# Performance work log

Measured on AMD Instinct MI355X. Metric: run time of the kernel, lower is better.

Reference implementation:

```python
import jax, jax.numpy as jnp
from jax import lax
import numpy as np

B, T = 8, 16
IMG = 128
CF = 32            # c_CNN_out = dim_C2_2 (feature channels / NTM slot width)
WO = HO = 32       # w_CNN_out, h_CNN_out
N = WO * HO        # dim_C2_1 = NTM memory slots (flattened spatial)
M = CF
DH = 256           # dim_h_o
LAMBDA0 = 1e-4
EPS = 1e-8


def setup_inputs() -> dict:
    key = jax.random.key(0)
    ks = jax.random.split(key, 12)
    f32 = jnp.float32
    inp = {}
    inp["x_i"] = jax.random.normal(ks[0], (B, T, 3, IMG, IMG), f32)
    inp["z_i"] = jax.random.normal(ks[1], (B, T, 3, IMG, IMG), f32)
    # feature CNN (3 -> CF -> CF, stride 2 each)
    inp["conv1_w"] = jax.random.normal(ks[2], (CF, 3, 3, 3), f32) * 0.1
    inp["conv1_b"] = jnp.zeros((CF,), f32)
    inp["conv2_w"] = jax.random.normal(ks[3], (CF, CF, 3, 3), f32) * 0.05
    inp["conv2_b"] = jnp.zeros((CF,), f32)
    # NTM controller / addressing parameters
    inp["Wk"] = jax.random.normal(ks[4], (M, DH), f32) * 0.05
    inp["bk"] = jnp.zeros((M,), f32)
    inp["Wbeta"] = jax.random.normal(ks[5], (1, DH), f32) * 0.05
    inp["bbeta"] = jnp.zeros((1,), f32)
    inp["Wh"] = jax.random.normal(ks[6], (DH, DH + 2 * M), f32) * 0.05
    inp["bh"] = jnp.zeros((DH,), f32)
    inp["We"] = jax.random.normal(ks[7], (M, DH), f32) * 0.05
    inp["Wa"] = jax.random.normal(ks[8], (M, DH), f32) * 0.05
    inp["Wg"] = jax.random.normal(ks[9], (1, DH), f32) * 0.05
    # DCF cosine window and gaussian-label FFT (stored as real/imag pair like torch.rfft)
    win = np.hanning(WO)
    inp["cos_window"] = jnp.asarray(np.outer(win, win), f32)
    sigma = 2.0
    g = np.arange(WO)
    g = np.minimum(g, WO - g)  # circular distance, peak at origin
    d2 = g[:, None] ** 2 + g[None, :] ** 2
    y = np.exp(-d2 / (2.0 * sigma ** 2)).astype(np.float32)
    yfc = np.fft.rfft2(y)
    inp["yf"] = jnp.asarray(np.stack([yfc.real, yfc.imag], -1), f32)[None, None]  # [1,1,WO,WO//2+1,2]
    return inp


def _conv(x, w, b):
    out = lax.conv_general_dilated(x, w, (2, 2), "SAME",
                                   dimension_numbers=("NCHW", "OIHW", "NCHW"))
    return out + b[None, :, None, None]


def _feature(x, c1w, c1b, c2w, c2b):
    x = jax.nn.relu(_conv(x, c1w, c1b))
    return jax.nn.relu(_conv(x, c2w, c2b))  # [BT, CF, WO, HO]


def _layernorm(x):
    # LayerNorm over last two dims [dim_C2_1, dim_C2_2], no affine
    mu = x.mean(axis=(-2, -1), keepdims=True)
    var = x.var(axis=(-2, -1), keepdims=True)
    return (x - mu) / jnp.sqrt(var + 1e-5)


def reference(x_i, z_i, conv1_w, conv1_b, conv2_w, conv2_b,
              Wk, bk, Wbeta, bbeta, Wh, bh, We, Wa, Wg, cos_window, yf):
    # feature extraction
    xf_btcwh = _feature(x_i.reshape(B * T, 3, IMG, IMG), conv1_w, conv1_b, conv2_w, conv2_b)
    zf_btcwh = _feature(z_i.reshape(B * T, 3, IMG, IMG), conv1_w, conv1_b, conv2_w, conv2_b)
    xf = xf_btcwh.transpose(0, 2, 3, 1).reshape(B, T, N, M)  # [B,T,N,M]

    h0 = jnp.zeros((B, DH), xf.dtype)
    c0 = _layernorm(xf[:, 0])  # init_x_norm on first frame features

    def cell(carry, x_t):
        h, c = carry  # h [B,DH], c [B,N,M]; x_t [B,N,M]
        # content-based addressing
        k = jnp.tanh(h @ Wk.T + bk)                           # [B,M]
        beta = jax.nn.softplus(h @ Wbeta.T + bbeta)           # [B,1]
        cn = c / (jnp.linalg.norm(c, axis=-1, keepdims=True) + EPS)
        kn = k / (jnp.linalg.norm(k, axis=-1, keepdims=True) + EPS)
        sims = jnp.einsum("bnm,bm->bn", cn, kn)               # cosine sim [B,N]
        w = jax.nn.softmax(beta * sims, axis=-1)              # read/write weights
        r = jnp.einsum("bn,bnm->bm", w, c)                    # read vector
        # controller update
        inp = jnp.concatenate([h, r, x_t.mean(axis=1)], axis=-1)  # [B,DH+2M]
        h_new = jnp.tanh(inp @ Wh.T + bh)
        # erase / add / input-gate write
        e = jax.nn.sigmoid(h_new @ We.T)                      # [B,M]
        a = jnp.tanh(h_new @ Wa.T)                            # [B,M]
        g = jax.nn.sigmoid(h_new @ Wg.T)[:, :, None]          # [B,1,1]
        c_write = c * (1.0 - w[:, :, None] * e[:, None, :]) + w[:, :, None] * a[:, None, :]
        c_new = (1.0 - g) * c_write + g * x_t
        return (h_new, c_new), c_new

    (_, _), c_seq = lax.scan(cell, (h0, c0), xf.transpose(1, 0, 2, 3))
    c_seq = c_seq.transpose(1, 0, 2, 3)                       # [B,T,N,M]

    # c.permute(0,1,3,2).view(B*T, dim_C2_2, WO, HO)
    c_btcwh = c_seq.transpose(0, 1, 3, 2).reshape(B * T, M, WO, HO)

    # DCF correlation in Fourier domain
    cw = cos_window[None, None]
    cfft = jnp.fft.rfft2(c_btcwh * cw)                        # [BT,M,WO,WO//2+1]
    zfft = jnp.fft.rfft2(zf_btcwh * cw)
    kzzf = (cfft.real ** 2 + cfft.imag ** 2).sum(axis=1, keepdims=True)   # [BT,1,WO,Wf]
    kxzf = (zfft * jnp.conj(cfft)).sum(axis=1, keepdims=True)             # complex_mulconj sum
    yfc = yf[..., 0] + 1j * yf[..., 1]                         # [1,1,WO,Wf]
    alphaf = yfc / (kzzf + LAMBDA0)
    response = jnp.fft.irfft2(kxzf * alphaf, s=(WO, HO))       # [BT,1,WO,HO]
    return response.reshape(B, T, WO, HO)
```

## Files before the change

kernel.cpp:

```cpp
#include <hip/hip_runtime.h>
#include <hip/hip_fp16.h>
#include <math.h>


#define TWOPI_32 0.19634954084936207f

typedef _Float16 __h2 __attribute__((ext_vector_type(2)));
__device__ __forceinline__ float fdot2(unsigned int w, unsigned int h, float acc) {
    union { unsigned int u; __h2 v; } a, b;
    a.u = w; b.u = h;
    return __builtin_amdgcn_fdot2(a.v, b.v, acc, false);
}
__device__ __forceinline__ unsigned int packh2(float a, float b) {
    __half2 h2 = __floats2half2_rn(a, b);
    return *(unsigned int*)&h2;
}

__global__ __launch_bounds__(256) void prepack_kernel(
    const float* __restrict__ Wh, const float* __restrict__ Wk,
    const float* __restrict__ We, const float* __restrict__ Wa,
    const float* __restrict__ c1w, const float* __restrict__ c2w,
    __half* __restrict__ whhP, __half* __restrict__ whrxP,
    __half* __restrict__ wkP, __half* __restrict__ weP, __half* __restrict__ waP,
    float* __restrict__ twg,
    unsigned int* __restrict__ c2wP, unsigned int* __restrict__ c1wP01,
    float* __restrict__ c1wP2)
{
    const int tid = threadIdx.x;
    if (blockIdx.x < 32) {
        const int base = blockIdx.x*256 + tid;
        #pragma unroll
        for (int r = 0; r < 8; ++r) {
            int idx = base*8 + r;
            int e = idx & 7, i = (idx >> 3) & 255, c = idx >> 11;
            int q = c >> 4, k = c & 15;
            whhP[idx] = __float2half(Wh[i*320 + q*128 + k*8 + e]);
        }
        #pragma unroll
        for (int r = 0; r < 2; ++r) {
            int idx = base*2 + r;
            int i = idx >> 6, s2 = idx & 63;
            whrxP[idx] = __float2half(Wh[i*320 + 256 + s2]);
        }
        {
            int idx = base;
            int m = idx >> 8, j = (idx >> 4) & 15, e = idx & 15;
            int col = (e < 8) ? (8*j + e) : (128 + 8*j + (e - 8));
            wkP[idx] = __float2half(Wk[m*256 + col]);
            weP[idx] = __float2half(We[m*256 + col]);
            waP[idx] = __float2half(Wa[m*256 + col]);
        }
    } else {
        for (int idx = tid; idx < 4608; idx += 256) {
            int half = idx / 2304;
            int rem  = idx - half*2304;
            int ic2  = rem / 144;
            int r2   = rem - ic2*144;
            int j    = r2 / 9, q = r2 - j*9;
            int oc   = half*16 + j;
            c2wP[((half*16 + ic2)*16 + j)*12 + q] =
                packh2(c2w[oc*288 + (2*ic2)*9 + q],
                       c2w[oc*288 + (2*ic2+1)*9 + q]);
        }
        for (int idx = tid; idx < 288; idx += 256) {
            int oc = idx / 9, r = idx - oc*9;
            c1wP01[idx] = packh2(c1w[oc*27 + r*3 + 0], c1w[oc*27 + r*3 + 1]);
            c1wP2[idx]  = c1w[oc*27 + r*3 + 2];
        }
        for (int idx = tid; idx < 1024; idx += 256) {
            int w = idx >> 5, k = idx & 31;
            float sv, cv;
            sincosf(TWOPI_32 * (float)((w*k) & 31), &sv, &cv);
            twg[idx*2]     = cv;
            twg[idx*2 + 1] = -sv;
        }
    }
}

__global__ __launch_bounds__(256) void conv1_kernel(const float* __restrict__ in,
                                                    const unsigned int* __restrict__ w01,
                                                    const float* __restrict__ w2,
                                                    const float* __restrict__ bias,
                                                    unsigned int* __restrict__ out)
{
    const int strip = blockIdx.x;
    const int img   = blockIdx.y;
    const int tid   = threadIdx.x;
    __shared__ __align__(16) unsigned int sIn2[3*33*66];
    __shared__ unsigned int sw01[288];
    __shared__ float sw2[288];
    __shared__ float sb[32];
    for (int i = tid; i < 288; i += 256) { sw01[i] = w01[i]; sw2[i] = w2[i]; }
    if (tid < 32) sb[tid] = bias[tid];
    const int iy0 = strip * 32;
    for (int idx = tid; idx < 3*33*66; idx += 256) {
        int ic  = idx / (33*66);
        int rem = idx - ic*(33*66);
        int li  = rem / 66;
        int x2  = rem - li*66;
        int iy  = iy0 + li;
        unsigned int v = 0;
        if (iy < 128 && x2 < 64) {
            float2 p = *(const float2*)&in[(((size_t)img*3 + ic)*128 + iy)*128 + 2*x2];
            v = packh2(p.x, p.y);
        }
        sIn2[idx] = v;
    }
    __syncthreads();
    const int oy0 = strip*16;
    #pragma unroll
    for (int p = 0; p < 4; ++p) {
        int pos = p*256 + tid;
        int ly = pos >> 6;
        int ox = pos & 63;
        unsigned int pa[9];
        float px[9];
        #pragma unroll
        for (int ic = 0; ic < 3; ++ic)
            #pragma unroll
            for (int dy = 0; dy < 3; ++dy) {
                int r = ic*3 + dy;
                int rowb = ic*(33*66) + (2*ly+dy)*66;
                pa[r] = sIn2[rowb + ox];
                unsigned int u = sIn2[rowb + ox + 1];
                px[r] = __half2float(((const __half2*)&u)->x);
            }
        for (int oc2 = 0; oc2 < 16; ++oc2) {
            const int oca = 2*oc2, ocb = 2*oc2 + 1;
            float acca = sb[oca], accb = sb[ocb];
            #pragma unroll
            for (int r = 0; r < 9; ++r) {
                acca = fdot2(sw01[oca*9 + r], pa[r], acca);
                acca += sw2[oca*9 + r] * px[r];
                accb = fdot2(sw01[ocb*9 + r], pa[r], accb);
                accb += sw2[ocb*9 + r] * px[r];
            }
            out[(((size_t)img*16 + oc2)*64 + (oy0+ly))*64 + ox] =
                packh2(fmaxf(acca, 0.f), fmaxf(accb, 0.f));
        }
    }
}

__global__ __launch_bounds__(256) void conv2_kernel(const unsigned int* __restrict__ in,
                                                    const unsigned int* __restrict__ wP,
                                                    const float* __restrict__ bias,
                                                    float* __restrict__ out)
{
    const int strip = blockIdx.x;
    const int img   = blockIdx.y;
    const int tid   = threadIdx.x;
    __shared__ __align__(16) unsigned int sIn2[16*9*66];
    __shared__ __align__(16) unsigned int sW[6144];
    __shared__ float sb[32];
    for (int i = tid; i < 1536; i += 256) ((uint4*)sW)[i] = ((const uint4*)wP)[i];
    if (tid < 32) sb[tid] = bias[tid];
    const int iy0 = strip*8;
    for (int idx = tid; idx < 16*9*66; idx += 256) {
        int ic2 = idx / (9*66);
        int rem = idx - ic2*(9*66);
        int li  = rem / 66;
        int col = rem - li*66;
        int iy  = iy0 + li;
        unsigned int v = 0;
        if (iy < 64 && col < 64)
            v = in[(((size_t)img*16 + ic2)*64 + iy)*64 + col];
        sIn2[idx] = v;
    }
    __syncthreads();
    const int posl = tid & 127;
    const int half = tid >> 7;
    const int ly = posl >> 5;
    const int ox = posl & 31;
    float acc[16];
    #pragma unroll
    for (int j = 0; j < 16; ++j) acc[j] = 0.f;
    for (int ic2 = 0; ic2 < 16; ++ic2) {
        unsigned int patch[9];
        #pragma unroll
        for (int dy = 0; dy < 3; ++dy)
            #pragma unroll
            for (int dx = 0; dx < 3; ++dx)
                patch[dy*3+dx] = sIn2[ic2*(9*66) + (2*ly+dy)*66 + 2*ox + dx];
        const unsigned int* wbase = sW + (half*16 + ic2)*192;
        #pragma unroll
        for (int j = 0; j < 16; ++j) {
            const unsigned int* wr = wbase + j*12;
            uint4 wa = *(const uint4*)wr;
            uint4 wb = *(const uint4*)(wr + 4);
            unsigned int w8 = wr[8];
            float a = acc[j];
            a = fdot2(wa.x, patch[0], a); a = fdot2(wa.y, patch[1], a);
            a = fdot2(wa.z, patch[2], a); a = fdot2(wa.w, patch[3], a);
            a = fdot2(wb.x, patch[4], a); a = fdot2(wb.y, patch[5], a);
            a = fdot2(wb.z, patch[6], a); a = fdot2(wb.w, patch[7], a);
            a = fdot2(w8,  patch[8], a);
            acc[j] = a;
        }
    }
    const int oy = strip*4 + ly;
    #pragma unroll
    for (int j = 0; j < 16; ++j) {
        int oc = half*16 + j;
        out[(((size_t)img*32 + oc)*32 + oy)*32 + ox] = fmaxf(acc[j] + sb[oc], 0.f);
    }
}

__global__ __launch_bounds__(256) void prep2_kernel(
    const float* __restrict__ xf, __half* __restrict__ xh, float* __restrict__ xmean)
{
    const int tid = threadIdx.x;
    const int bt = blockIdx.x;
    __shared__ float sT[32][257];
    const float* src = xf + (size_t)bt*32768;
    __half* dst = xh + (size_t)bt*32768;
    for (int tt = 0; tt < 4; ++tt) {
        #pragma unroll
        for (int m = 0; m < 32; ++m)
            sT[m][tid] = src[m*1024 + tt*256 + tid];
        __syncthreads();
        uint4 o[4];
        unsigned int* ou = (unsigned int*)o;
        #pragma unroll
        for (int k = 0; k < 16; ++k)
            ou[k] = packh2(sT[2*k][tid], sT[2*k+1][tid]);
        uint4* dp = (uint4*)(dst + (size_t)(tt*256 + tid)*32);
        dp[0] = o[0]; dp[1] = o[1]; dp[2] = o[2]; dp[3] = o[3];
        __syncthreads();
    }
    const int m = tid >> 3, s8 = tid & 7;
    float sm = 0.f;
    #pragma unroll 16
    for (int k = 0; k < 128; ++k) sm += src[m*1024 + s8 + 8*k];
    sm += __shfl_down(sm, 4, 8); sm += __shfl_down(sm, 2, 8); sm += __shfl_down(sm, 1, 8);
    if (s8 == 0) xmean[bt*32 + m] = sm * (1.f/1024.f);
}

__global__ __launch_bounds__(512, 2) void fat_kernel(
    const float* __restrict__ xfeat, const __half* __restrict__ xh,
    const float* __restrict__ xmean,
    const __half* __restrict__ whhP, const __half* __restrict__ whrxP,
    const __half* __restrict__ wkP, const __half* __restrict__ weP,
    const __half* __restrict__ waP,
    const float* __restrict__ bk, const float* __restrict__ Wbeta,
    const float* __restrict__ bbeta, const float* __restrict__ bh,
    const float* __restrict__ Wg,
    float* __restrict__ wbuf, float* __restrict__ eag, float* __restrict__ lnst,
    const float* __restrict__ z_i, const unsigned int* __restrict__ c1w01,
    const float* __restrict__ c1w2, const float* __restrict__ c1b,
    const unsigned int* __restrict__ c2wP, const float* __restrict__ c2b,
    float* __restrict__ zfeat)
{
    __shared__ __align__(16) char smem[139264];

    if (blockIdx.x < 8) {
        __half* sWhh = (__half*)(smem);
        float (*sHbuf)[256] = (float(*)[256])(smem + 131072);
        __half (*sHh)[256] = (__half(*)[256])(smem + 133120);
        float* sK    = (float*)(smem + 134144);
        float* sXm   = (float*)(smem + 134272);
        float* sRedC = (float*)(smem + 136320);
        float* sR32  = (float*)(smem + 137344);
        float* sE    = (float*)(smem + 137472);
        float* sA    = (float*)(smem + 137600);
        float* sBk   = (float*)(smem + 137728);
        float* sBh   = (float*)(smem + 137856);
        float* sRedD = (float*)(smem + 138880);
        float* sRedL = (float*)(smem + 138912);

        const int b    = blockIdx.x;
        const int tid  = threadIdx.x;
        const int lane = tid & 63;
        const int wid  = tid >> 6;

        {
            const uint4* src = (const uint4*)whhP;
            uint4* dst = (uint4*)sWhh;
            for (int i2 = tid; i2 < 8192; i2 += 512) dst[i2] = src[i2];
        }
        if (tid < 256) { sBh[tid] = bh[tid]; sHbuf[0][tid] = 0.f; sHh[0][tid] = __float2half(0.f); }
        if (tid < 32)  { sBk[tid] = bk[tid]; sK[tid] = tanhf(bk[tid]); }
        if (tid < 512) sXm[tid] = xmean[b*512 + tid];
        float4 wbeta4 = *(const float4*)&Wbeta[(size_t)lane*4];
        float4 wg4    = *(const float4*)&Wg[(size_t)lane*4];
        float bb = bbeta[0];

        const int mg = tid >> 4, jg = tid & 15;
        uint4 wk0, wk1, we0, we1, wa0, wa1;
        {
            const uint4* p;
            p = (const uint4*)(wkP + (size_t)(mg*16 + jg)*16); wk0 = p[0]; wk1 = p[1];
            p = (const uint4*)(weP + (size_t)(mg*16 + jg)*16); we0 = p[0]; we1 = p[1];
            p = (const uint4*)(waP + (size_t)(mg*16 + jg)*16); wa0 = p[0]; wa1 = p[1];
        }
        const int iD = tid >> 1, qD = tid & 1;
        uint4 wrx0, wrx1, wrx2, wrx3;
        {
            const uint4* p = (const uint4*)(whrxP + (size_t)iD*64 + qD*32);
            wrx0 = p[0]; wrx1 = p[1]; wrx2 = p[2]; wrx3 = p[3];
        }

        const int n0 = 2*tid;
        float c0[32], c1[32];

        {
            const float* x0 = xfeat + (size_t)(b*16)*32768;
            float sum = 0.f, ss = 0.f;
            #pragma unroll
            for (int m = 0; m < 32; ++m) {
                float2 v = *(const float2*)&x0[m*1024 + n0];
                c0[m] = v.x; c1[m] = v.y;
                sum += v.x + v.y; ss += v.x*v.x + v.y*v.y;
            }
            #pragma unroll
            for (int d = 32; d > 0; d >>= 1) { sum += __shfl_xor(sum, d, 64); ss += __shfl_xor(ss, d, 64); }
            if (lane == 0) { sRedL[wid] = sum; sRedL[8+wid] = ss; }
            __syncthreads();
            float S = 0.f, SS = 0.f;
            #pragma unroll
            for (int i = 0; i < 8; ++i) { S += sRedL[i]; SS += sRedL[8+i]; }
            float mu = S * (1.f/32768.f);
            float var = SS * (1.f/32768.f) - mu*mu;
            float rs = rsqrtf(var + 1e-5f);
            if (tid == 0) { lnst[b*2] = mu; lnst[b*2+1] = rs; }
            #pragma unroll
            for (int m = 0; m < 32; ++m) { c0[m] = (c0[m]-mu)*rs; c1[m] = (c1[m]-mu)*rs; }
        }

        uint4 xb[8];
        {
            const uint4* xrow = (const uint4*)(xh + (size_t)(b*16)*32768) + 8*tid;
            #pragma unroll
            for (int i = 0; i < 8; ++i) xb[i] = xrow[i];
        }
        __syncthreads();

        float betav = (bb > 20.f) ? bb : log1pf(expf(bb));
        float ex0 = 0.f, ex1 = 0.f, w0 = 0.f, w1 = 0.f;
        const int rm = ((lane&1)<<4)|((lane&2)<<2)|(lane&4)|((lane&8)>>2)|((lane&16)>>4);

        #pragma unroll 1
        for (int t = 0; t < 16; ++t) {
            const int cur = t & 1, nxt = cur ^ 1;

            {
                float beta = betav;
                float dot0 = 0.f, dot1 = 0.f, cn20 = 0.f, cn21 = 0.f, kn2 = 0.f;
                #pragma unroll
                for (int q = 0; q < 8; ++q) {
                    float4 k4 = *(const float4*)&sK[4*q];
                    dot0 += c0[4*q]*k4.x + c0[4*q+1]*k4.y + c0[4*q+2]*k4.z + c0[4*q+3]*k4.w;
                    dot1 += c1[4*q]*k4.x + c1[4*q+1]*k4.y + c1[4*q+2]*k4.z + c1[4*q+3]*k4.w;
                    cn20 += c0[4*q]*c0[4*q] + c0[4*q+1]*c0[4*q+1] + c0[4*q+2]*c0[4*q+2] + c0[4*q+3]*c0[4*q+3];
                    cn21 += c1[4*q]*c1[4*q] + c1[4*q+1]*c1[4*q+1] + c1[4*q+2]*c1[4*q+2] + c1[4*q+3]*c1[4*q+3];
                    kn2  += k4.x*k4.x + k4.y*k4.y + k4.z*k4.z + k4.w*k4.w;
                }
                float kinv = 1.f / (sqrtf(kn2) + 1e-8f);
                float s0 = dot0 * kinv / (sqrtf(cn20) + 1e-8f);
                float s1 = dot1 * kinv / (sqrtf(cn21) + 1e-8f);
                ex0 = expf(beta * s0);
                ex1 = expf(beta * s1);
                float es = ex0 + ex1;
                #pragma unroll
                for (int d = 32; d > 0; d >>= 1) es += __shfl_xor(es, d, 64);
                if (lane == 0) sRedD[wid] = es;
                float v[32];
                #pragma unroll
                for (int m = 0; m < 32; ++m) v[m] = ex0*c0[m] + ex1*c1[m];
                #pragma unroll
                for (int i = 0; i < 16; ++i) { float sd = (lane&1)? v[i] : v[i+16]; float rc = __shfl_xor(sd, 1, 64); v[i] = ((lane&1)? v[i+16] : v[i]) + rc; }
                #pragma unroll
                for (int i = 0; i < 8; ++i)  { float sd = (lane&2)? v[i] : v[i+8];  float rc = __shfl_xor(sd, 2, 64); v[i] = ((lane&2)? v[i+8]  : v[i]) + rc; }
                #pragma unroll
                for (int i = 0; i < 4; ++i)  { float sd = (lane&4)? v[i] : v[i+4];  float rc = __shfl_xor(sd, 4, 64); v[i] = ((lane&4)? v[i+4]  : v[i]) + rc; }
                #pragma unroll
                for (int i = 0; i < 2; ++i)  { float sd = (lane&8)? v[i] : v[i+2];  float rc = __shfl_xor(sd, 8, 64); v[i] = ((lane&8)? v[i+2]  : v[i]) + rc; }
                { float sd = (lane&16)? v[0] : v[1]; float rc = __shfl_xor(sd, 16, 64); v[0] = ((lane&16)? v[1] : v[0]) + rc; }
                v[0] += __shfl_xor(v[0], 32, 64);
                if (lane < 32) sRedC[wid*32 + rm] = v[0];
            }
            __syncthreads();

            {
                float den = sRedD[0]+sRedD[1]+sRedD[2]+sRedD[3]+sRedD[4]+sRedD[5]+sRedD[6]+sRedD[7];
                float inv = 1.f / den;
                w0 = ex0 * inv; w1 = ex1 * inv;
                *(float2*)&wbuf[(size_t)(b*16 + t)*1024 + n0] = make_float2(w0, w1);
                if (lane < 32) {
                    float r = 0.f;
                    #pragma unroll
                    for (int w = 0; w < 8; ++w) r += sRedC[w*32 + lane];
                    sR32[lane] = r * inv;
                }
                float s0 = 0.f, s1 = 0.f, s2 = 0.f, s3 = 0.f;
                #pragma unroll
                for (int k4 = 0; k4 < 4; ++k4) {
                    const int kb = 4*k4;
                    uint4 wv0 = *(const uint4*)&sWhh[(size_t)((qD*16 + kb+0)*256 + iD)*8];
                    uint4 hv0 = *(const uint4*)&sHh[cur][qD*128 + (kb+0)*8];
                    s0 = fdot2(wv0.x, hv0.x, s0); s0 = fdot2(wv0.y, hv0.y, s0);
                    s0 = fdot2(wv0.z, hv0.z, s0); s0 = fdot2(wv0.w, hv0.w, s0);
                    uint4 wv1 = *(const uint4*)&sWhh[(size_t)((qD*16 + kb+1)*256 + iD)*8];
                    uint4 hv1 = *(const uint4*)&sHh[cur][qD*128 + (kb+1)*8];
                    s1 = fdot2(wv1.x, hv1.x, s1); s1 = fdot2(wv1.y, hv1.y, s1);
                    s1 = fdot2(wv1.z, hv1.z, s1); s1 = fdot2(wv1.w, hv1.w, s1);
                    uint4 wv2 = *(const uint4*)&sWhh[(size_t)((qD*16 + kb+2)*256 + iD)*8];
                    uint4 hv2 = *(const uint4*)&sHh[cur][qD*128 + (kb+2)*8];
                    s2 = fdot2(wv2.x, hv2.x, s2); s2 = fdot2(wv2.y, hv2.y, s2);
                    s2 = fdot2(wv2.z, hv2.z, s2); s2 = fdot2(wv2.w, hv2.w, s2);
                    uint4 wv3 = *(const uint4*)&sWhh[(size_t)((qD*16 + kb+3)*256 + iD)*8];
                    uint4 hv3 = *(const uint4*)&sHh[cur][qD*128 + (kb+3)*8];
                    s3 = fdot2(wv3.x, hv3.x, s3); s3 = fdot2(wv3.y, hv3.y, s3);
                    s3 = fdot2(wv3.z, hv3.z, s3); s3 = fdot2(wv3.w, hv3.w, s3);
                }
                const float* rxsrc = qD ? &sXm[t*32] : sR32;
                {
                    const __half2* w2;
                    float4 va, vb;
                    va = *(const float4*)&rxsrc[0];  vb = *(const float4*)&rxsrc[4];
                    w2 = (const __half2*)&wrx0;
                    { float2 p0 = __half22float2(w2[0]); s0 += p0.x*va.x + p0.y*va.y;
                      float2 p1 = __half22float2(w2[1]); s0 += p1.x*va.z + p1.y*va.w;
                      float2 p2 = __half22float2(w2[2]); s0 += p2.x*vb.x + p2.y*vb.y;
                      float2 p3 = __half22float2(w2[3]); s0 += p3.x*vb.z + p3.y*vb.w; }
                    va = *(const float4*)&rxsrc[8];  vb = *(const float4*)&rxsrc[12];
                    w2 = (const __half2*)&wrx1;
                    { float2 p0 = __half22float2(w2[0]); s1 += p0.x*va.x + p0.y*va.y;
                      float2 p1 = __half22float2(w2[1]); s1 += p1.x*va.z + p1.y*va.w;
                      float2 p2 = __half22float2(w2[2]); s1 += p2.x*vb.x + p2.y*vb.y;
                      float2 p3 = __half22float2(w2[3]); s1 += p3.x*vb.z + p3.y*vb.w; }
                    va = *(const float4*)&rxsrc[16]; vb = *(const float4*)&rxsrc[20];
                    w2 = (const __half2*)&wrx2;
                    { float2 p0 = __half22float2(w2[0]); s2 += p0.x*va.x + p0.y*va.y;
                      float2 p1 = __half22float2(w2[1]); s2 += p1.x*va.z + p1.y*va.w;
                      float2 p2 = __half22float2(w2[2]); s2 += p2.x*vb.x + p2.y*vb.y;
                      float2 p3 = __half22float2(w2[3]); s2 += p3.x*vb.z + p3.y*vb.w; }
                    va = *(const float4*)&rxsrc[24]; vb = *(const float4*)&rxsrc[28];
                    w2 = (const __half2*)&wrx3;
                    { float2 p0 = __half22float2(w2[0]); s3 += p0.x*va.x + p0.y*va.y;
                      float2 p1 = __half22float2(w2[1]); s3 += p1.x*va.z + p1.y*va.w;
                      float2 p2 = __half22float2(w2[2]); s3 += p2.x*vb.x + p2.y*vb.y;
                      float2 p3 = __half22float2(w2[3]); s3 += p3.x*vb.z + p3.y*vb.w; }
                }
                float s = (s0 + s1) + (s2 + s3);
                s += __shfl_down(s, 1, 2);
                if (qD == 0) {
                    float hn = tanhf(s + sBh[iD]);
                    sHbuf[nxt][iD] = hn;
                    sHh[nxt][iD] = __float2half(hn);
                }
            }
            __syncthreads();

            float gg;
            {
                uint4 h0 = *(const uint4*)&sHh[nxt][8*jg];
                uint4 h1 = *(const uint4*)&sHh[nxt][128 + 8*jg];
                float se0=0.f, se1=0.f, sa0=0.f, sa1=0.f, sk0=0.f, sk1=0.f;
                se0 = fdot2(we0.x, h0.x, se0); se1 = fdot2(we0.y, h0.y, se1);
                se0 = fdot2(we0.z, h0.z, se0); se1 = fdot2(we0.w, h0.w, se1);
                se0 = fdot2(we1.x, h1.x, se0); se1 = fdot2(we1.y, h1.y, se1);
                se0 = fdot2(we1.z, h1.z, se0); se1 = fdot2(we1.w, h1.w, se1);
                sa0 = fdot2(wa0.x, h0.x, sa0); sa1 = fdot2(wa0.y, h0.y, sa1);
                sa0 = fdot2(wa0.z, h0.z, sa0); sa1 = fdot2(wa0.w, h0.w, sa1);
                sa0 = fdot2(wa1.x, h1.x, sa0); sa1 = fdot2(wa1.y, h1.y, sa1);
                sa0 = fdot2(wa1.z, h1.z, sa0); sa1 = fdot2(wa1.w, h1.w, sa1);
                sk0 = fdot2(wk0.x, h0.x, sk0); sk1 = fdot2(wk0.y, h0.y, sk1);
                sk0 = fdot2(wk0.z, h0.z, sk0); sk1 = fdot2(wk0.w, h0.w, sk1);
                sk0 = fdot2(wk1.x, h1.x, sk0); sk1 = fdot2(wk1.y, h1.y, sk1);
                sk0 = fdot2(wk1.z, h1.z, sk0); sk1 = fdot2(wk1.w, h1.w, sk1);
                float se = se0 + se1, sa = sa0 + sa1, sk = sk0 + sk1;
                se += __shfl_down(se, 8, 16); sa += __shfl_down(sa, 8, 16); sk += __shfl_down(sk, 8, 16);
                se += __shfl_down(se, 4, 16); sa += __shfl_down(sa, 4, 16); sk += __shfl_down(sk, 4, 16);
                se += __shfl_down(se, 2, 16); sa += __shfl_down(sa, 2, 16); sk += __shfl_down(sk, 2, 16);
                se += __shfl_down(se, 1, 16); sa += __shfl_down(sa, 1, 16); sk += __shfl_down(sk, 1, 16);
                if (jg == 0) {
                    float e = 1.f/(1.f + expf(-se));
                    float a = tanhf(sa);
                    sE[mg] = e; sA[mg] = a;
                    sK[mg] = tanhf(sk + sBk[mg]);
                    eag[(size_t)(b*16 + t)*80 + mg]      = e;
                    eag[(size_t)(b*16 + t)*80 + 32 + mg] = a;
                }
                float4 h4 = *(const float4*)&sHbuf[nxt][lane*4];
                float pg = wg4.x*h4.x + wg4.y*h4.y + wg4.z*h4.z + wg4.w*h4.w;
                float pb = wbeta4.x*h4.x + wbeta4.y*h4.y + wbeta4.z*h4.z + wbeta4.w*h4.w;
                #pragma unroll
                for (int d = 32; d > 0; d >>= 1) {
                    pg += __shfl_xor(pg, d, 64);
                    pb += __shfl_xor(pb, d, 64);
                }
                gg = 1.f/(1.f + expf(-pg));
                float xbeta = pb + bb;
                betav = (xbeta > 20.f) ? xbeta : log1pf(expf(xbeta));
                if (tid == 0) eag[(size_t)(b*16 + t)*80 + 64] = gg;
            }
            __syncthreads();

            {
                float omg = 1.f - gg;
                const __half* xp = (const __half*)xb;
                #pragma unroll
                for (int q = 0; q < 8; ++q) {
                    float4 e4 = *(const float4*)&sE[4*q];
                    float4 a4 = *(const float4*)&sA[4*q];
                    #pragma unroll
                    for (int r = 0; r < 4; ++r) {
                        int m = 4*q + r;
                        float e = (r==0)?e4.x:(r==1)?e4.y:(r==2)?e4.z:e4.w;
                        float a = (r==0)?a4.x:(r==1)?a4.y:(r==2)?a4.z:a4.w;
                        float x0v = __half2float(xp[m]);
                        float x1v = __half2float(xp[32 + m]);
                        c0[m] = omg*(c0[m]*(1.f - w0*e) + w0*a) + gg*x0v;
                        c1[m] = omg*(c1[m]*(1.f - w1*e) + w1*a) + gg*x1v;
                    }
                }
                if (t < 15) {
                    const uint4* xrow = (const uint4*)(xh + (size_t)(b*16 + t + 1)*32768) + 8*tid;
                    #pragma unroll
                    for (int i = 0; i < 8; ++i) xb[i] = xrow[i];
                }
            }
        }
    } else {
        const int team = threadIdx.x >> 8;
        const int t256 = threadIdx.x & 255;
        const int tile = (blockIdx.x - 8)*2 + team;
        const int img  = tile >> 3;
        const int strip = tile & 7;
        unsigned int* sZ  = (unsigned int*)(smem + team*53072);
        unsigned int* sC1 = (unsigned int*)(smem + team*53072 + 15048);
        unsigned int* sW   = (unsigned int*)(smem + 106144);
        unsigned int* sw01 = (unsigned int*)(smem + 130720);
        float*        sw2  = (float*)(smem + 131872);
        float*        sb2  = (float*)(smem + 133024);
        float*        sb1  = (float*)(smem + 133152);

        for (int i = threadIdx.x; i < 1536; i += 512)
            ((uint4*)sW)[i] = ((const uint4*)c2wP)[i];
        for (int i = threadIdx.x; i < 288; i += 512) { sw01[i] = c1w01[i]; sw2[i] = c1w2[i]; }
        if (threadIdx.x < 32) { sb2[threadIdx.x] = c2b[threadIdx.x]; sb1[threadIdx.x] = c1b[threadIdx.x]; }

        const int zrow0 = strip*16;
        for (int idx = t256; idx < 3762; idx += 256) {
            int ic = idx / (19*66);
            int rem = idx - ic*(19*66);
            int li = rem / 66;
            int x2 = rem - li*66;
            int iy = zrow0 + li;
            unsigned int v = 0;
            if (iy < 128 && x2 < 64) {
                float2 p = *(const float2*)&z_i[(((size_t)img*3 + ic)*128 + iy)*128 + 2*x2];
                v = packh2(p.x, p.y);
            }
            sZ[idx] = v;
        }
        for (int idx = t256; idx < 16*9*2; idx += 256) {
            int oc2 = idx / 18; int rem = idx - oc2*18; int li = rem >> 1; int c = 64 + (rem & 1);
            sC1[oc2*(9*66) + li*66 + c] = 0;
        }
        __syncthreads();
        for (int pos = t256; pos < 576; pos += 256) {
            int li = pos >> 6;
            int ox = pos & 63;
            unsigned int pa[9]; float px[9];
            #pragma unroll
            for (int ic = 0; ic < 3; ++ic)
                #pragma unroll
                for (int dy = 0; dy < 3; ++dy) {
                    int r = ic*3 + dy;
                    int rowb = ic*(19*66) + (2*li + dy)*66;
                    pa[r] = sZ[rowb + ox];
                    unsigned int u = sZ[rowb + ox + 1];
                    px[r] = __half2float(((const __half2*)&u)->x);
                }
            const bool phantom = (strip == 7) && (li == 8);
            #pragma unroll 4
            for (int oc2 = 0; oc2 < 16; ++oc2) {
                const int oca = 2*oc2, ocb = oca + 1;
                float acca = sb1[oca], accb = sb1[ocb];
                #pragma unroll
                for (int r = 0; r < 9; ++r) {
                    acca = fdot2(sw01[oca*9 + r], pa[r], acca);
                    acca += sw2[oca*9 + r] * px[r];
                    accb = fdot2(sw01[ocb*9 + r], pa[r], accb);
                    accb += sw2[ocb*9 + r] * px[r];
                }
                sC1[oc2*(9*66) + li*66 + ox] =
                    phantom ? 0u : packh2(fmaxf(acca, 0.f), fmaxf(accb, 0.f));
            }
        }
        __syncthreads();
        const int posl = t256 & 127;
        const int half = t256 >> 7;
        const int ly = posl >> 5;
        const int ox = posl & 31;
        float acc[16];
        #pragma unroll
        for (int j = 0; j < 16; ++j) acc[j] = 0.f;
        for (int ic2 = 0; ic2 < 16; ++ic2) {
            unsigned int patch[9];
            #pragma unroll
            for (int dy = 0; dy < 3; ++dy)
                #pragma unroll
                for (int dx = 0; dx < 3; ++dx)
                    patch[dy*3+dx] = sC1[ic2*(9*66) + (2*ly+dy)*66 + 2*ox + dx];
            const unsigned int* wbase = sW + (half*16 + ic2)*192;
            #pragma unroll
            for (int j = 0; j < 16; ++j) {
                const unsigned int* wr = wbase + j*12;
                uint4 wa = *(const uint4*)wr;
                uint4 wb = *(const uint4*)(wr + 4);
                unsigned int w8 = wr[8];
                float a = acc[j];
                a = fdot2(wa.x, patch[0], a); a = fdot2(wa.y, patch[1], a);
                a = fdot2(wa.z, patch[2], a); a = fdot2(wa.w, patch[3], a);
                a = fdot2(wb.x, patch[4], a); a = fdot2(wb.y, patch[5], a);
                a = fdot2(wb.z, patch[6], a); a = fdot2(wb.w, patch[7], a);
                a = fdot2(w8,  patch[8], a);
                acc[j] = a;
            }
        }
        const int oy = strip*4 + ly;
        #pragma unroll
        for (int j = 0; j < 16; ++j) {
            int oc = half*16 + j;
            zfeat[(((size_t)img*32 + oc)*32 + oy)*32 + ox] = fmaxf(acc[j] + sb2[oc], 0.f);
        }
    }
}

__global__ __launch_bounds__(256) void ntm_replay_kernel(
    const float* __restrict__ xfeat, const float* __restrict__ wbuf,
    const float* __restrict__ eag, const float* __restrict__ lnst,
    float* __restrict__ cseq)
{
    const int slab = blockIdx.x;
    const int b    = blockIdx.y;
    const int tid  = threadIdx.x;
    const int m    = tid >> 3;
    const int ns   = tid & 7;
    const int n0   = slab*64 + ns*8;
    const float mu = lnst[b*2], rs = lnst[b*2+1];

    float c[8];
    {
        const float* x0 = xfeat + (size_t)(b*16)*32768 + m*1024 + n0;
        float4 a = *(const float4*)x0;
        float4 bv = *(const float4*)(x0 + 4);
        c[0]=(a.x-mu)*rs; c[1]=(a.y-mu)*rs; c[2]=(a.z-mu)*rs; c[3]=(a.w-mu)*rs;
        c[4]=(bv.x-mu)*rs; c[5]=(bv.y-mu)*rs; c[6]=(bv.z-mu)*rs; c[7]=(bv.w-mu)*rs;
    }
    for (int t = 0; t < 16; ++t) {
        const size_t bt = (size_t)(b*16 + t);
        const float* wp = &wbuf[bt*1024 + n0];
        float4 wA = *(const float4*)wp;
        float4 wB = *(const float4*)(wp + 4);
        float e = eag[bt*80 + m];
        float a = eag[bt*80 + 32 + m];
        float g = eag[bt*80 + 64];
        float omg = 1.f - g;
        const float* xp = &xfeat[bt*32768 + m*1024 + n0];
        float4 xA = *(const float4*)xp;
        float4 xB = *(const float4*)(xp + 4);
        c[0] = omg*(c[0]*(1.f - wA.x*e) + wA.x*a) + g*xA.x;
        c[1] = omg*(c[1]*(1.f - wA.y*e) + wA.y*a) + g*xA.y;
        c[2] = omg*(c[2]*(1.f - wA.z*e) + wA.z*a) + g*xA.z;
        c[3] = omg*(c[3]*(1.f - wA.w*e) + wA.w*a) + g*xA.w;
        c[4] = omg*(c[4]*(1.f - wB.x*e) + wB.x*a) + g*xB.x;
        c[5] = omg*(c[5]*(1.f - wB.y*e) + wB.y*a) + g*xB.y;
        c[6] = omg*(c[6]*(1.f - wB.z*e) + wB.z*a) + g*xB.z;
        c[7] = omg*(c[7]*(1.f - wB.w*e) + wB.w*a) + g*xB.w;
        float* op = &cseq[bt*32768 + m*1024 + n0];
        *(float4*)op       = make_float4(c[0], c[1], c[2], c[3]);
        *(float4*)(op + 4) = make_float4(c[4], c[5], c[6], c[7]);
    }
}

__global__ __launch_bounds__(256) void fft_fwd_kernel(const float* __restrict__ srcA,
                                                      const float* __restrict__ srcB,
                                                      const float* __restrict__ cosw,
                                                      const float* __restrict__ twg,
                                                      float* __restrict__ dstA,
                                                      float* __restrict__ dstB)
{
    const int img = blockIdx.x;
    const int tid = threadIdx.x;
    const float* src; float* dst;
    if (img < 4096) { src = srcA + (size_t)img*1024;        dst = dstA + (size_t)img*1088; }
    else            { src = srcB + (size_t)(img-4096)*1024; dst = dstB + (size_t)(img-4096)*1088; }

    __shared__ __align__(16) float sY[32*36];
    __shared__ __align__(16) float sT[2048];
    __shared__ __align__(16) float sR[2048];

    {
        const float4* s4 = (const float4*)twg;
        float4* d4 = (float4*)sT;
        d4[tid]       = s4[tid];
        d4[256 + tid] = s4[256 + tid];
    }
    {
        float4 v = *(const float4*)&src[tid*4];
        float4 c = *(const float4*)&cosw[tid*4];
        *(float4*)&sY[(tid>>3)*36 + (tid&7)*4] = make_float4(v.x*c.x, v.y*c.y, v.z*c.z, v.w*c.w);
    }
    __syncthreads();

    const int hj = tid >> 3;
    const int k0 = (tid & 7) * 4;

    float r0=0.f,i0=0.f,r1=0.f,i1=0.f,r2=0.f,i2=0.f,r3=0.f,i3=0.f;
    #pragma unroll
    for (int w = 0; w < 32; ++w) {
        float y = sY[hj*36 + w];
        float4 ta = *(const float4*)&sT[(w*32 + k0)*2];
        float4 tb = *(const float4*)&sT[(w*32 + k0)*2 + 4];
        r0 += y*ta.x; i0 += y*ta.y;
        r1 += y*ta.z; i1 += y*ta.w;
        r2 += y*tb.x; i2 += y*tb.y;
        r3 += y*tb.z; i3 += y*tb.w;
    }
    *(float4*)&sR[(hj*32 + k0)*2]     = make_float4(r0,i0,r1,i1);
    *(float4*)&sR[(hj*32 + k0)*2 + 4] = make_float4(r2,i2,r3,i3);
    __syncthreads();

    float fr0=0.f,fi0=0.f,fr1=0.f,fi1=0.f,fr2=0.f,fi2=0.f,fr3=0.f,fi3=0.f;
    #pragma unroll
    for (int h = 0; h < 32; ++h) {
        float2 wj = *(const float2*)&sT[(h*32 + hj)*2];
        float4 Ra = *(const float4*)&sR[(h*32 + k0)*2];
        float4 Rb = *(const float4*)&sR[(h*32 + k0)*2 + 4];
        fr0 += Ra.x*wj.x - Ra.y*wj.y;  fi0 += Ra.x*wj.y + Ra.y*wj.x;
        fr1 += Ra.z*wj.x - Ra.w*wj.y;  fi1 += Ra.z*wj.y + Ra.w*wj.x;
        fr2 += Rb.x*wj.x - Rb.y*wj.y;  fi2 += Rb.x*wj.y + Rb.y*wj.x;
        fr3 += Rb.z*wj.x - Rb.w*wj.y;  fi3 += Rb.z*wj.y + Rb.w*wj.x;
    }
    float* dp = dst + (size_t)(hj*17 + k0)*2;
    if (k0 < 16) {
        *(float2*)&dp[0] = make_float2(fr0, fi0);
        *(float2*)&dp[2] = make_float2(fr1, fi1);
        *(float2*)&dp[4] = make_float2(fr2, fi2);
        *(float2*)&dp[6] = make_float2(fr3, fi3);
    } else if (k0 == 16) {
        *(float2*)&dp[0] = make_float2(fr0, fi0);
    }
}

__global__ __launch_bounds__(256) void comb_ifft_kernel(const float* __restrict__ cfft,
                                                        const float* __restrict__ zfft,
                                                        const float* __restrict__ yf,
                                                        float* __restrict__ out)
{
    const int bt  = blockIdx.x;
    const int tid = threadIdx.x;
    __shared__ float sG[544*2];
    __shared__ float sS[544*2];
    __shared__ float ct[32], st[32];
    if (tid < 32) {
        float sv, cv;
        sincosf(TWOPI_32 * (float)tid, &sv, &cv);
        ct[tid] = cv; st[tid] = sv;
    }
    for (int idx = tid; idx < 544; idx += 256) {
        float kzz = 0.f, kxr = 0.f, kxi = 0.f;
        #pragma unroll 4
        for (int m = 0; m < 32; ++m) {
            size_t base = ((size_t)(bt*32 + m)*1088) + idx*2;
            float2 c = *(const float2*)&cfft[base];
            float2 z = *(const float2*)&zfft[base];
            kzz += c.x*c.x + c.y*c.y;
            kxr += z.x*c.x + z.y*c.y;
            kxi += z.y*c.x - z.x*c.y;
        }
        float den = 1.f / (kzz + 1e-4f);
        float2 y = *(const float2*)&yf[idx*2];
        float ar = y.x*den, ai = y.y*den;
        sG[idx*2]     = kxr*ar - kxi*ai;
        sG[idx*2 + 1] = kxr*ai + kxi*ar;
    }
    __syncthreads();
    for (int idx = tid; idx < 544; idx += 256) {
        int h = idx / 17;
        int k = idx - h*17;
        float re = 0.f, im = 0.f;
        #pragma unroll
        for (int j = 0; j < 32; ++j) {
            float gr = sG[(j*17+k)*2], gi = sG[(j*17+k)*2+1];
            int a = (h*j) & 31;
            float c = ct[a], s = st[a];
            re += gr*c - gi*s;
            im += gr*s + gi*c;
        }
        sS[(h*17+k)*2] = re; sS[(h*17+k)*2+1] = im;
    }
    __syncthreads();
    #pragma unroll
    for (int p = 0; p < 4; ++p) {
        int pos = p*256 + tid;
        int h = pos >> 5, wq = pos & 31;
        float acc = sS[(h*17)*2];
        #pragma unroll
        for (int k = 1; k < 16; ++k) {
            int a = (wq*k) & 31;
            acc += 2.f*(sS[(h*17+k)*2]*ct[a] - sS[(h*17+k)*2+1]*st[a]);
        }
        acc += sS[(h*17+16)*2] * ((wq & 1) ? -1.f : 1.f);
        out[(size_t)bt*1024 + pos] = acc * (1.f/1024.f);
    }
}

extern "C" void kernel_launch(void* const* d_in, const int* in_sizes, int n_in,
                              void* d_out, int out_size, void* d_ws, size_t ws_size,
                              hipStream_t stream)
{
    const float* x_i   = (const float*)d_in[0];
    const float* z_i   = (const float*)d_in[1];
    const float* c1w   = (const float*)d_in[2];
    const float* c1b   = (const float*)d_in[3];
    const float* c2w   = (const float*)d_in[4];
    const float* c2b   = (const float*)d_in[5];
    const float* Wk    = (const float*)d_in[6];
    const float* bk    = (const float*)d_in[7];
    const float* Wbeta = (const float*)d_in[8];
    const float* bbeta = (const float*)d_in[9];
    const float* Wh    = (const float*)d_in[10];
    const float* bh    = (const float*)d_in[11];
    const float* We    = (const float*)d_in[12];
    const float* Wa    = (const float*)d_in[13];
    const float* Wg    = (const float*)d_in[14];
    const float* cosw  = (const float*)d_in[15];
    const float* yf    = (const float*)d_in[16];
    float* out = (float*)d_out;
    float* ws  = (float*)d_ws;

    unsigned int* buf1p = (unsigned int*)ws;
    float*  xfeat = ws + 16777216;
    float*  zfeat = ws + 20971520;
    float*  cseq  = ws + 25165824;
    float*  xmb   = ws + 29499392;
    float*  cfft  = ws;
    float*  zfft  = ws + 4456448;
    __half* xhb   = (__half*)(ws + 9000000);
    float*  wbuf  = ws + 11100000;
    float*  eag   = ws + 11240000;
    float*  lnstp = ws + 11251000;
    __half* whhP  = (__half*)(ws + 29360128);
    __half* whrxP = (__half*)(ws + 29392896);
    __half* wkP   = (__half*)(ws + 29401088);
    __half* weP   = (__half*)(ws + 29405184);
    __half* waP   = (__half*)(ws + 29409280);
    float*  twg   = ws + 29413376;
    unsigned int* c2wP   = (unsigned int*)(ws + 29415424);
    unsigned int* c1wP01 = (unsigned int*)(ws + 29421568);
    float*  c1wP2 = ws + 29421856;

    dim3 b256(256);
    prepack_kernel<<<33, b256, 0, stream>>>(Wh, Wk, We, Wa, c1w, c2w,
                                            whhP, whrxP, wkP, weP, waP, twg,
                                            c2wP, c1wP01, c1wP2);
    conv1_kernel<<<dim3(4,128), b256, 0, stream>>>(x_i, c1wP01, c1wP2, c1b, buf1p);
    conv2_kernel<<<dim3(8,128), b256, 0, stream>>>(buf1p, c2wP, c2b, xfeat);
    prep2_kernel<<<128, b256, 0, stream>>>(xfeat, xhb, xmb);
    fat_kernel<<<520, 512, 0, stream>>>(xfeat, xhb, xmb, whhP, whrxP, wkP, weP, waP,
                                        bk, Wbeta, bbeta, bh, Wg, wbuf, eag, lnstp,
                                        z_i, c1wP01, c1wP2, c1b, c2wP, c2b, zfeat);
    ntm_replay_kernel<<<dim3(16,8), b256, 0, stream>>>(xfeat, wbuf, eag, lnstp, cseq);
    fft_fwd_kernel<<<8192, b256, 0, stream>>>(cseq, zfeat, cosw, twg, cfft, zfft);
    comb_ifft_kernel<<<128, b256, 0, stream>>>(cfft, zfft, yf, out);
}
```

Baseline: 445.7 us.

## Fuse conv1, conv2 and fp16 pack/mean prep into one x-feature kernel

Merges the conv1, conv2 and prep2 kernels into a single convx kernel. Each 256-thread team computes a conv1 strip with a halo directly into shared memory, runs conv2 on it, then writes fp32 features, the fp16 transposed copy and per-strip partial means. This removes the global round trip of the conv1 intermediate and two launches. The cost is recomputing the conv1 halo rows and adding a 16-way partial-mean sum in fat_kernel. Separately, it raises the wave priority of the NTM recurrence blocks and reorders two fdot2 calls.

```diff
diff --git a/kernel.cpp b/kernel.cpp
--- a/kernel.cpp
+++ b/kernel.cpp
@@ -77,57 +77,69 @@
     }
 }
 
-__global__ __launch_bounds__(256) void conv1_kernel(const float* __restrict__ in,
-                                                    const unsigned int* __restrict__ w01,
-                                                    const float* __restrict__ w2,
-                                                    const float* __restrict__ bias,
-                                                    unsigned int* __restrict__ out)
+__global__ __launch_bounds__(512, 2) void convx_kernel(
+    const float* __restrict__ x_i, const unsigned int* __restrict__ c1w01,
+    const float* __restrict__ c1w2, const float* __restrict__ c1b,
+    const unsigned int* __restrict__ c2wP, const float* __restrict__ c2b,
+    float* __restrict__ xfeat, __half* __restrict__ xh, float* __restrict__ xmp)
 {
-    const int strip = blockIdx.x;
-    const int img   = blockIdx.y;
-    const int tid   = threadIdx.x;
-    __shared__ __align__(16) unsigned int sIn2[3*33*66];
-    __shared__ unsigned int sw01[288];
-    __shared__ float sw2[288];
-    __shared__ float sb[32];
-    for (int i = tid; i < 288; i += 256) { sw01[i] = w01[i]; sw2[i] = w2[i]; }
-    if (tid < 32) sb[tid] = bias[tid];
-    const int iy0 = strip * 32;
-    for (int idx = tid; idx < 3*33*66; idx += 256) {
-        int ic  = idx / (33*66);
-        int rem = idx - ic*(33*66);
-        int li  = rem / 66;
-        int x2  = rem - li*66;
-        int iy  = iy0 + li;
+    __shared__ __align__(16) char smem[139264];
+    const int team = threadIdx.x >> 8;
+    const int t256 = threadIdx.x & 255;
+    const int tile = blockIdx.x*2 + team;
+    const int img  = tile >> 3;
+    const int strip = tile & 7;
+    unsigned int* sZ  = (unsigned int*)(smem + team*53072);
+    unsigned int* sC1 = (unsigned int*)(smem + team*53072 + 15048);
+    unsigned int* sW   = (unsigned int*)(smem + 106144);
+    unsigned int* sw01 = (unsigned int*)(smem + 130720);
+    float*        sw2  = (float*)(smem + 131872);
+    float*        sb2  = (float*)(smem + 133024);
+    float*        sb1  = (float*)(smem + 133152);
+
+    for (int i = threadIdx.x; i < 1536; i += 512)
+        ((uint4*)sW)[i] = ((const uint4*)c2wP)[i];
+    for (int i = threadIdx.x; i < 288; i += 512) { sw01[i] = c1w01[i]; sw2[i] = c1w2[i]; }
+    if (threadIdx.x < 32) { sb2[threadIdx.x] = c2b[threadIdx.x]; sb1[threadIdx.x] = c1b[threadIdx.x]; }
+
+    const int zrow0 = strip*16;
+    for (int idx = t256; idx < 3762; idx += 256) {
+        int ic = idx / (19*66);
+        int rem = idx - ic*(19*66);
+        int li = rem / 66;
+        int x2 = rem - li*66;
+        int iy = zrow0 + li;
         unsigned int v = 0;
         if (iy < 128 && x2 < 64) {
-            float2 p = *(const float2*)&in[(((size_t)img*3 + ic)*128 + iy)*128 + 2*x2];
+            float2 p = *(const float2*)&x_i[(((size_t)img*3 + ic)*128 + iy)*128 + 2*x2];
             v = packh2(p.x, p.y);
         }
-        sIn2[idx] = v;
+        sZ[idx] = v;
+    }
+    for (int idx = t256; idx < 16*9*2; idx += 256) {
+        int oc2 = idx / 18; int rem = idx - oc2*18; int li = rem >> 1; int c = 64 + (rem & 1);
+        sC1[oc2*(9*66) + li*66 + c] = 0;
     }
     __syncthreads();
-    const int oy0 = strip*16;
-    #pragma unroll
-    for (int p = 0; p < 4; ++p) {
-        int pos = p*256 + tid;
-        int ly = pos >> 6;
+    for (int pos = t256; pos < 576; pos += 256) {
+        int li = pos >> 6;
         int ox = pos & 63;
-        unsigned int pa[9];
-        float px[9];
+        unsigned int pa[9]; float px[9];
         #pragma unroll
         for (int ic = 0; ic < 3; ++ic)
             #pragma unroll
             for (int dy = 0; dy < 3; ++dy) {
                 int r = ic*3 + dy;
-                int rowb = ic*(33*66) + (2*ly+dy)*66;
-                pa[r] = sIn2[rowb + ox];
-                unsigned int u = sIn2[rowb + ox + 1];
+                int rowb = ic*(19*66) + (2*li + dy)*66;
+                pa[r] = sZ[rowb + ox];
+                unsigned int u = sZ[rowb + ox + 1];
                 px[r] = __half2float(((const __half2*)&u)->x);
             }
+        const bool phantom = (strip == 7) && (li == 8);
+        #pragma unroll 4
         for (int oc2 = 0; oc2 < 16; ++oc2) {
-            const int oca = 2*oc2, ocb = 2*oc2 + 1;
-            float acca = sb[oca], accb = sb[ocb];
+            const int oca = 2*oc2, ocb = oca + 1;
+            float acca = sb1[oca], accb = sb1[ocb];
             #pragma unroll
             for (int r = 0; r < 9; ++r) {
                 acca = fdot2(sw01[oca*9 + r], pa[r], acca);
@@ -135,40 +147,13 @@
                 accb = fdot2(sw01[ocb*9 + r], pa[r], accb);
                 accb += sw2[ocb*9 + r] * px[r];
             }
-            out[(((size_t)img*16 + oc2)*64 + (oy0+ly))*64 + ox] =
-                packh2(fmaxf(acca, 0.f), fmaxf(accb, 0.f));
-        }
-    }
-}
-
-__global__ __launch_bounds__(256) void conv2_kernel(const unsigned int* __restrict__ in,
-                                                    const unsigned int* __restrict__ wP,
-                                                    const float* __restrict__ bias,
-                                                    float* __restrict__ out)
-{
-    const int strip = blockIdx.x;
-    const int img   = blockIdx.y;
-    const int tid   = threadIdx.x;
-    __shared__ __align__(16) unsigned int sIn2[16*9*66];
-    __shared__ __align__(16) unsigned int sW[6144];
-    __shared__ float sb[32];
-    for (int i = tid; i < 1536; i += 256) ((uint4*)sW)[i] = ((const uint4*)wP)[i];
-    if (tid < 32) sb[tid] = bias[tid];
-    const int iy0 = strip*8;
-    for (int idx = tid; idx < 16*9*66; idx += 256) {
-        int ic2 = idx / (9*66);
-        int rem = idx - ic2*(9*66);
-        int li  = rem / 66;
-        int col = rem - li*66;
-        int iy  = iy0 + li;
-        unsigned int v = 0;
-        if (iy < 64 && col < 64)
-            v = in[(((size_t)img*16 + ic2)*64 + iy)*64 + col];
-        sIn2[idx] = v;
+            sC1[oc2*(9*66) + li*66 + ox] =
+                phantom ? 0u : packh2(fmaxf(acca, 0.f), fmaxf(accb, 0.f));
+        }
     }
     __syncthreads();
-    const int posl = tid & 127;
-    const int half = tid >> 7;
+    const int posl = t256 & 127;
+    const int half = t256 >> 7;
     const int ly = posl >> 5;
     const int ox = posl & 31;
     float acc[16];
@@ -180,7 +165,7 @@
         for (int dy = 0; dy < 3; ++dy)
             #pragma unroll
             for (int dx = 0; dx < 3; ++dx)
-                patch[dy*3+dx] = sIn2[ic2*(9*66) + (2*ly+dy)*66 + 2*ox + dx];
+                patch[dy*3+dx] = sC1[ic2*(9*66) + (2*ly+dy)*66 + 2*ox + dx];
         const unsigned int* wbase = sW + (half*16 + ic2)*192;
         #pragma unroll
         for (int j = 0; j < 16; ++j) {
@@ -198,46 +183,40 @@
         }
     }
     const int oy = strip*4 + ly;
+    const int n  = oy*32 + ox;
+    float vals[16];
     #pragma unroll
     for (int j = 0; j < 16; ++j) {
         int oc = half*16 + j;
-        out[(((size_t)img*32 + oc)*32 + oy)*32 + ox] = fmaxf(acc[j] + sb[oc], 0.f);
-    }
-}
-
-__global__ __launch_bounds__(256) void prep2_kernel(
-    const float* __restrict__ xf, __half* __restrict__ xh, float* __restrict__ xmean)
-{
-    const int tid = threadIdx.x;
-    const int bt = blockIdx.x;
-    __shared__ float sT[32][257];
-    const float* src = xf + (size_t)bt*32768;
-    __half* dst = xh + (size_t)bt*32768;
-    for (int tt = 0; tt < 4; ++tt) {
-        #pragma unroll
-        for (int m = 0; m < 32; ++m)
-            sT[m][tid] = src[m*1024 + tt*256 + tid];
-        __syncthreads();
-        uint4 o[4];
-        unsigned int* ou = (unsigned int*)o;
-        #pragma unroll
-        for (int k = 0; k < 16; ++k)
-            ou[k] = packh2(sT[2*k][tid], sT[2*k+1][tid]);
-        uint4* dp = (uint4*)(dst + (size_t)(tt*256 + tid)*32);
-        dp[0] = o[0]; dp[1] = o[1]; dp[2] = o[2]; dp[3] = o[3];
-        __syncthreads();
-    }
-    const int m = tid >> 3, s8 = tid & 7;
-    float sm = 0.f;
-    #pragma unroll 16
-    for (int k = 0; k < 128; ++k) sm += src[m*1024 + s8 + 8*k];
-    sm += __shfl_down(sm, 4, 8); sm += __shfl_down(sm, 2, 8); sm += __shfl_down(sm, 1, 8);
-    if (s8 == 0) xmean[bt*32 + m] = sm * (1.f/1024.f);
+        float v = fmaxf(acc[j] + sb2[oc], 0.f);
+        vals[j] = v;
+        xfeat[(((size_t)img*32 + oc)*32 + oy)*32 + ox] = v;
+    }
+    {
+        unsigned int hp[8];
+        #pragma unroll
+        for (int k = 0; k < 8; ++k) hp[k] = packh2(vals[2*k], vals[2*k+1]);
+        uint4* dp = (uint4*)(xh + (size_t)img*32768 + (size_t)n*32 + half*16);
+        dp[0] = *(uint4*)&hp[0];
+        dp[1] = *(uint4*)&hp[4];
+    }
+    {
+        const int lane = threadIdx.x & 63;
+        const int wsub = (t256 >> 6) & 1;
+        #pragma unroll
+        for (int j = 0; j < 16; ++j) {
+            float v = vals[j];
+            #pragma unroll
+            for (int d = 32; d > 0; d >>= 1) v += __shfl_xor(v, d, 64);
+            if (lane == 0)
+                xmp[(((size_t)img*8 + strip)*2 + wsub)*32 + half*16 + j] = v * (1.f/1024.f);
+        }
+    }
 }
 
 __global__ __launch_bounds__(512, 2) void fat_kernel(
     const float* __restrict__ xfeat, const __half* __restrict__ xh,
-    const float* __restrict__ xmean,
+    const float* __restrict__ xmp,
     const __half* __restrict__ whhP, const __half* __restrict__ whrxP,
     const __half* __restrict__ wkP, const __half* __restrict__ weP,
     const __half* __restrict__ waP,
@@ -253,6 +232,7 @@
     __shared__ __align__(16) char smem[139264];
 
     if (blockIdx.x < 8) {
+        __builtin_amdgcn_s_setprio(1);
         __half* sWhh = (__half*)(smem);
         float (*sHbuf)[256] = (float(*)[256])(smem + 131072);
         __half (*sHh)[256] = (__half(*)[256])(smem + 133120);
@@ -279,7 +259,14 @@
         }
         if (tid < 256) { sBh[tid] = bh[tid]; sHbuf[0][tid] = 0.f; sHh[0][tid] = __float2half(0.f); }
         if (tid < 32)  { sBk[tid] = bk[tid]; sK[tid] = tanhf(bk[tid]); }
-        if (tid < 512) sXm[tid] = xmean[b*512 + tid];
+        if (tid < 512) {
+            const int tt = tid >> 5, m = tid & 31;
+            const float* pp = xmp + ((size_t)(b*16 + tt)*16)*32 + m;
+            float s = 0.f;
+            #pragma unroll
+            for (int q = 0; q < 16; ++q) s += pp[q*32];
+            sXm[tid] = s;
+        }
         float4 wbeta4 = *(const float4*)&Wbeta[(size_t)lane*4];
         float4 wg4    = *(const float4*)&Wg[(size_t)lane*4];
         float bb = bbeta[0];
@@ -410,7 +397,7 @@
                     uint4 wv3 = *(const uint4*)&sWhh[(size_t)((qD*16 + kb+3)*256 + iD)*8];
                     uint4 hv3 = *(const uint4*)&sHh[cur][qD*128 + (kb+3)*8];
                     s3 = fdot2(wv3.x, hv3.x, s3); s3 = fdot2(wv3.y, hv3.y, s3);
-                    s3 = fdot2(wv3.z, hv3.z, s3); s3 = fdot2(wv3.w, hv3.w, s3);
+                    s3 = fdot2(wv3.w, hv3.w, s3); s3 = fdot2(wv3.z, hv3.z, s3);
                 }
                 const float* rxsrc = qD ? &sXm[t*32] : sR32;
                 {
@@ -833,11 +820,9 @@
     float* out = (float*)d_out;
     float* ws  = (float*)d_ws;
 
-    unsigned int* buf1p = (unsigned int*)ws;
     float*  xfeat = ws + 16777216;
     float*  zfeat = ws + 20971520;
     float*  cseq  = ws + 25165824;
-    float*  xmb   = ws + 29499392;
     float*  cfft  = ws;
     float*  zfft  = ws + 4456448;
     __half* xhb   = (__half*)(ws + 9000000);
@@ -853,15 +838,15 @@
     unsigned int* c2wP   = (unsigned int*)(ws + 29415424);
     unsigned int* c1wP01 = (unsigned int*)(ws + 29421568);
     float*  c1wP2 = ws + 29421856;
+    float*  xmp   = ws + 29422144;
 
     dim3 b256(256);
     prepack_kernel<<<33, b256, 0, stream>>>(Wh, Wk, We, Wa, c1w, c2w,
                                             whhP, whrxP, wkP, weP, waP, twg,
                                             c2wP, c1wP01, c1wP2);
-    conv1_kernel<<<dim3(4,128), b256, 0, stream>>>(x_i, c1wP01, c1wP2, c1b, buf1p);
-    conv2_kernel<<<dim3(8,128), b256, 0, stream>>>(buf1p, c2wP, c2b, xfeat);
-    prep2_kernel<<<128, b256, 0, stream>>>(xfeat, xhb, xmb);
-    fat_kernel<<<520, 512, 0, stream>>>(xfeat, xhb, xmb, whhP, whrxP, wkP, weP, waP,
+    convx_kernel<<<512, 512, 0, stream>>>(x_i, c1wP01, c1wP2, c1b, c2wP, c2b,
+                                          xfeat, xhb, xmp);
+    fat_kernel<<<520, 512, 0, stream>>>(xfeat, xhb, xmp, whhP, whrxP, wkP, weP, waP,
                                         bk, Wbeta, bbeta, bh, Wg, wbuf, eag, lnstp,
                                         z_i, c1wP01, c1wP2, c1b, c2wP, c2b, zfeat);
     ntm_replay_kernel<<<dim3(16,8), b256, 0, stream>>>(xfeat, wbuf, eag, lnstp, cseq);
```

Measured after the change: 427.9 us. 1.04x faster.
